# Optimization experiments

Hardware: AMD Instinct MI355X
Metric: run time of the kernel (lower is better)

The kernel has to match this reference:

```python
import jax, jax.numpy as jnp
import numpy as np

CLAMP_LO, CLAMP_HI, CLAMP_GATE_MAX = -10.0, 10.0, 10.0
E, TOPK = 8, 2
M, K, N = 2048, 2048, 1408  # tokens, hidden_dim, intermediate_dim
CAPACITY = 2 * (M * TOPK // E)


def setup_inputs() -> dict:
    key = jax.random.key(0)
    ks = jax.random.split(key, 6)
    bk = 1.0 / np.sqrt(K)  # kaiming_uniform(a=sqrt(5)) bound = 1/sqrt(fan_in)
    bn = 1.0 / np.sqrt(N)
    return {
        "flat_h": jax.random.normal(ks[0], (M, K), jnp.float32),
        "flat_idx": jax.random.randint(ks[1], (M, TOPK), 0, E),
        "flat_gate": jax.random.uniform(ks[2], (M, TOPK), jnp.float32),
        "gate_weight": jax.random.uniform(ks[3], (E, N, K), jnp.float32, -bk, bk),
        "up_weight": jax.random.uniform(ks[4], (E, N, K), jnp.float32, -bk, bk),
        "down_weight": jax.random.uniform(ks[5], (E, K, N), jnp.float32, -bn, bn),
    }


def reference(flat_h, flat_idx, flat_gate, gate_weight, up_weight, down_weight):
    m, top_k = flat_idx.shape
    k = flat_h.shape[1]
    e = gate_weight.shape[0]
    r = m * top_k

    expert_id = flat_idx.reshape(-1)                                   # (R,)
    gate = flat_gate.reshape(-1)                                       # (R,)
    token_index = jnp.repeat(jnp.arange(m, dtype=jnp.int32), top_k)    # (R,)

    # stable sort rows by expert id (mirrors torch.argsort(..., stable=True))
    sort_idx = jnp.argsort(expert_id, stable=True)
    sorted_eid = expert_id[sort_idx]
    tok_sorted = token_index[sort_idx]
    gate_sorted = gate[sort_idx]

    # position of each sorted row inside its expert group
    counts = jnp.bincount(expert_id, length=e)
    starts = jnp.concatenate([jnp.zeros(1, counts.dtype), jnp.cumsum(counts)[:-1]])
    pos = jnp.arange(r) - starts[sorted_eid]                           # (R,)

    # dispatch: scatter sorted tokens into fixed-capacity (E, C, K) buffer
    buf = jnp.zeros((e, CAPACITY, k), flat_h.dtype)
    buf = buf.at[sorted_eid, pos].set(flat_h[tok_sorted])

    # grouped GEMMs: weights stored (E, out, in) like nn.Linear
    g = jnp.einsum("eck,enk->ecn", buf, gate_weight)
    g = jnp.minimum(g, CLAMP_GATE_MAX)
    u = jnp.clip(jnp.einsum("eck,enk->ecn", buf, up_weight), CLAMP_LO, CLAMP_HI)
    h = jax.nn.silu(g) * u                                             # SwiGLU (E, C, N)
    d = jnp.einsum("ecn,ekn->eck", h, down_weight)                     # (E, C, K)

    # combine: gather each routed row back, weight by gate, sum over top_k slots
    expert_out = d[sorted_eid, pos]                                    # (R, K)
    weighted = expert_out * gate_sorted[:, None]
    out = jnp.zeros((m, k), flat_h.dtype).at[tok_sorted].add(weighted)
    return out
```

## Files before the change

### kernel.cpp

```cpp
#include <hip/hip_runtime.h>

#define M_TOK 2048
#define KDIM 2048
#define NDIM 1408
#define NEXP 8
#define RROWS (M_TOK * 2)
#define CAP 1024

typedef __attribute__((ext_vector_type(8))) short short8;
typedef __attribute__((ext_vector_type(4))) float f32x4;

__device__ __forceinline__ unsigned short bf16rn(float f) {
    unsigned int u = __builtin_bit_cast(unsigned int, f);
    u += 0x7FFFu + ((u >> 16) & 1u);
    return (unsigned short)(u >> 16);
}
__device__ __forceinline__ unsigned int pk2(float a, float b) {
    return (unsigned int)bf16rn(a) | ((unsigned int)bf16rn(b) << 16);
}

__device__ __forceinline__ void glds16(const void* g, void* l) {
    __builtin_amdgcn_global_load_lds(
        (const __attribute__((address_space(1))) unsigned int*)g,
        (__attribute__((address_space(3))) unsigned int*)l, 16, 0, 0);
}

__global__ void k_route(const float* __restrict__ h, const int* __restrict__ idx,
                        int* __restrict__ cnt, int* __restrict__ slot_of,
                        unsigned short* __restrict__ bufA) {
    int r = blockIdx.x;
    __shared__ int s_ep;
    if (threadIdx.x == 0) {
        int e = idx[r];
        int p = atomicAdd(&cnt[e], 1);
        int ep = e * CAP + p;
        slot_of[r] = ep;
        s_ep = ep;
    }
    __syncthreads();
    int ep = s_ep;
    const float4* src = (const float4*)(h + (size_t)(r >> 1) * KDIM) + threadIdx.x * 2;
    float4 a = src[0], b = src[1];
    uint4 o;
    o.x = pk2(a.x, a.y); o.y = pk2(a.z, a.w);
    o.z = pk2(b.x, b.y); o.w = pk2(b.z, b.w);
    *((uint4*)(bufA + (size_t)ep * KDIM) + threadIdx.x) = o;
}

__global__ void k_cvt3(const float* __restrict__ s0, const float* __restrict__ s1,
                       const float* __restrict__ s2,
                       unsigned short* __restrict__ d0, unsigned short* __restrict__ d1,
                       unsigned short* __restrict__ d2) {
    const float* src = blockIdx.y == 0 ? s0 : (blockIdx.y == 1 ? s1 : s2);
    unsigned short* dst = blockIdx.y == 0 ? d0 : (blockIdx.y == 1 ? d1 : d2);
    int i = blockIdx.x * blockDim.x + threadIdx.x;
    const float4* s = (const float4*)src + (size_t)i * 2;
    float4 a = s[0], b = s[1];
    uint4 o;
    o.x = pk2(a.x, a.y); o.y = pk2(a.z, a.w);
    o.z = pk2(b.x, b.y); o.w = pk2(b.z, b.w);
    ((uint4*)dst)[i] = o;
}

__global__ __launch_bounds__(256, 2)
void k_gemm1(const unsigned short* __restrict__ bufA,
             const unsigned short* __restrict__ gwb,
             const unsigned short* __restrict__ uwb,
             const int* __restrict__ cnt, unsigned short* __restrict__ hbuf) {
    const int f = blockIdx.x;
    const int e = f & 7;
    const int t = f >> 3;
    const int n_blk = t % 11;
    const int m_blk = t / 11;
    const int m0 = m_blk * 128;
    if (m0 >= cnt[e]) return;
    const int n0 = n_blk * 128;

    const unsigned short* A = bufA + (size_t)e * CAP * KDIM;
    const unsigned short* G = gwb + (size_t)e * NDIM * KDIM;
    const unsigned short* U = uwb + (size_t)e * NDIM * KDIM;

    __shared__ unsigned short sA[128 * 64];
    __shared__ unsigned short sG[128 * 64];
    __shared__ unsigned short sU[128 * 64];

    const int tid = threadIdx.x;
    const int lane = tid & 63;
    const int wave = tid >> 6;
    const int wm = (wave >> 1) * 64, wn = (wave & 1) * 64;
    const int q = lane >> 4, l15 = lane & 15;
    const int sr = lane >> 3;
    const int scb = (lane & 7) ^ (sr & 7);
    const int xi = l15 & 7;
    const int cbl0 = (q ^ xi) * 8;
    const int cbl1 = ((4 + q) ^ xi) * 8;

    f32x4 accG[4][4] = {};
    f32x4 accU[4][4] = {};

    for (int k0 = 0; k0 < KDIM; k0 += 64) {
        __syncthreads();
#pragma unroll
        for (int c = 0; c < 4; c++) {
            int seg = wave * 4 + c;
            int row = seg * 8 + sr;
            glds16(A + (size_t)(m0 + row) * KDIM + k0 + scb * 8, &sA[seg * 512]);
            glds16(G + (size_t)(n0 + row) * KDIM + k0 + scb * 8, &sG[seg * 512]);
            glds16(U + (size_t)(n0 + row) * KDIM + k0 + scb * 8, &sU[seg * 512]);
        }
        __syncthreads();

#pragma unroll
        for (int kh = 0; kh < 2; kh++) {
            const int co = kh ? cbl1 : cbl0;
            short8 af[4], gf[4], uf[4];
#pragma unroll
            for (int i = 0; i < 4; i++) {
                af[i] = *(const short8*)&sA[(wm + i * 16 + l15) * 64 + co];
                gf[i] = *(const short8*)&sG[(wn + i * 16 + l15) * 64 + co];
                uf[i] = *(const short8*)&sU[(wn + i * 16 + l15) * 64 + co];
            }
#pragma unroll
            for (int i = 0; i < 4; i++)
#pragma unroll
                for (int j = 0; j < 4; j++) {
                    accG[i][j] = __builtin_amdgcn_mfma_f32_16x16x32_bf16(af[i], gf[j], accG[i][j], 0, 0, 0);
                    accU[i][j] = __builtin_amdgcn_mfma_f32_16x16x32_bf16(af[i], uf[j], accU[i][j], 0, 0, 0);
                }
        }
    }

    unsigned short* H = hbuf + (size_t)e * CAP * NDIM;
#pragma unroll
    for (int i = 0; i < 4; i++)
#pragma unroll
        for (int j = 0; j < 4; j++) {
            int col = n0 + wn + j * 16 + l15;
#pragma unroll
            for (int rg = 0; rg < 4; rg++) {
                int row = m0 + wm + i * 16 + q * 4 + rg;
                float g = accG[i][j][rg];
                float u = accU[i][j][rg];
                g = fminf(g, 10.f);
                u = fminf(fmaxf(u, -10.f), 10.f);
                float hv = g / (1.f + __expf(-g)) * u;
                H[(size_t)row * NDIM + col] = bf16rn(hv);
            }
        }
}

__global__ __launch_bounds__(256, 2)
void k_gemm2(const unsigned short* __restrict__ hbuf,
             const unsigned short* __restrict__ dwb, const int* __restrict__ cnt,
             float* __restrict__ dbuf) {
    const int f = blockIdx.x;
    const int e = f & 7;
    const int t = f >> 3;
    const int n_blk = t & 15;
    const int m_blk = t >> 4;
    const int cnt_e = cnt[e];
    const int m0 = m_blk * 128;
    if (m0 >= cnt_e) return;
    const int n0 = n_blk * 128;

    const unsigned short* A = hbuf + (size_t)e * CAP * NDIM;
    const unsigned short* B = dwb + (size_t)e * KDIM * NDIM;

    __shared__ unsigned short sA[128 * 64];
    __shared__ unsigned short sB[128 * 64];

    const int tid = threadIdx.x;
    const int lane = tid & 63;
    const int wave = tid >> 6;
    const int wm = (wave >> 1) * 64, wn = (wave & 1) * 64;
    const int q = lane >> 4, l15 = lane & 15;
    const int sr = lane >> 3;
    const int scb = (lane & 7) ^ (sr & 7);
    const int xi = l15 & 7;
    const int cbl0 = (q ^ xi) * 8;
    const int cbl1 = ((4 + q) ^ xi) * 8;

    f32x4 acc[4][4] = {};

    for (int k0 = 0; k0 < NDIM; k0 += 64) {
        __syncthreads();
#pragma unroll
        for (int c = 0; c < 4; c++) {
            int seg = wave * 4 + c;
            int row = seg * 8 + sr;
            glds16(A + (size_t)(m0 + row) * NDIM + k0 + scb * 8, &sA[seg * 512]);
            glds16(B + (size_t)(n0 + row) * NDIM + k0 + scb * 8, &sB[seg * 512]);
        }
        __syncthreads();

#pragma unroll
        for (int kh = 0; kh < 2; kh++) {
            const int co = kh ? cbl1 : cbl0;
            short8 af[4], bfr[4];
#pragma unroll
            for (int i = 0; i < 4; i++) {
                af[i] = *(const short8*)&sA[(wm + i * 16 + l15) * 64 + co];
                bfr[i] = *(const short8*)&sB[(wn + i * 16 + l15) * 64 + co];
            }
#pragma unroll
            for (int i = 0; i < 4; i++)
#pragma unroll
                for (int j = 0; j < 4; j++)
                    acc[i][j] = __builtin_amdgcn_mfma_f32_16x16x32_bf16(af[i], bfr[j], acc[i][j], 0, 0, 0);
        }
    }

    float* D = dbuf + (size_t)e * CAP * KDIM;
#pragma unroll
    for (int i = 0; i < 4; i++) {
#pragma unroll
        for (int rg = 0; rg < 4; rg++) {
            int row = m0 + wm + i * 16 + q * 4 + rg;
            if (row < cnt_e) {
                float* drow = D + (size_t)row * KDIM + n0 + wn + l15;
#pragma unroll
                for (int j = 0; j < 4; j++)
                    drow[j * 16] = acc[i][j][rg];
            }
        }
    }
}

__global__ void k_combine(const float* __restrict__ dbuf, const int* __restrict__ slot_of,
                          const float* __restrict__ gate, float* __restrict__ out) {
    int tk = blockIdx.x;
    int s0 = slot_of[2 * tk], s1 = slot_of[2 * tk + 1];
    float g0 = gate[2 * tk], g1 = gate[2 * tk + 1];
    const float4* r0 = (const float4*)(dbuf + (size_t)s0 * KDIM);
    const float4* r1 = (const float4*)(dbuf + (size_t)s1 * KDIM);
    float4* o = (float4*)(out + (size_t)tk * KDIM);
    int i = threadIdx.x * 2;
#pragma unroll
    for (int c = 0; c < 2; c++) {
        float4 a = r0[i + c], b = r1[i + c];
        float4 v;
        v.x = g0 * a.x + g1 * b.x;
        v.y = g0 * a.y + g1 * b.y;
        v.z = g0 * a.z + g1 * b.z;
        v.w = g0 * a.w + g1 * b.w;
        o[i + c] = v;
    }
}

extern "C" void kernel_launch(void* const* d_in, const int* in_sizes, int n_in,
                              void* d_out, int out_size, void* d_ws, size_t ws_size,
                              hipStream_t stream) {
    const float* flat_h = (const float*)d_in[0];
    const int* flat_idx = (const int*)d_in[1];
    const float* flat_gate = (const float*)d_in[2];
    const float* gw = (const float*)d_in[3];
    const float* uw = (const float*)d_in[4];
    const float* dwn = (const float*)d_in[5];
    float* out = (float*)d_out;

    char* w = (char*)d_ws;
    int* cnt = (int*)w;
    int* slot_of = (int*)(w + 256);
    unsigned short* bufA = (unsigned short*)(w + 1048576ull);
    unsigned short* hbuf = (unsigned short*)(w + 34603008ull);
    unsigned short* gwb  = (unsigned short*)(w + 57671680ull);
    unsigned short* uwb  = (unsigned short*)(w + 103809024ull);
    unsigned short* dwb  = (unsigned short*)(w + 149946368ull);
    float* dbuf = (float*)(w + 57671680ull);

    hipMemsetAsync(cnt, 0, 256, stream);

    const int welems8 = NEXP * NDIM * KDIM / 8;
    k_cvt3<<<dim3(welems8 / 256, 3), 256, 0, stream>>>(gw, uw, dwn, gwb, uwb, dwb);
    k_route<<<RROWS, 256, 0, stream>>>(flat_h, flat_idx, cnt, slot_of, bufA);
    k_gemm1<<<8 * 11 * 8, 256, 0, stream>>>(bufA, gwb, uwb, cnt, hbuf);
    k_gemm2<<<8 * 16 * 8, 256, 0, stream>>>(hbuf, dwb, cnt, dbuf);
    k_combine<<<M_TOK, 256, 0, stream>>>(dbuf, slot_of, flat_gate, out);
}
```

Before: 462.2 us.

## Fuse fp32-to-bf16 weight conversion into grouped GEMM tile loads

Removes the standalone weight conversion kernel and has both GEMM kernels load fp32 weights directly, converting to bf16 in registers before writing swizzled tiles to LDS. This avoids a full read-write pass over all expert weights. In exchange, each m-block reads fp32 weights (double the bytes per reuse), loses the async global-to-LDS path for weights, and raises register pressure.

```diff
diff --git a/kernel.cpp b/kernel.cpp
--- a/kernel.cpp
+++ b/kernel.cpp
@@ -1,4 +1,5 @@
 #include <hip/hip_runtime.h>
+#include <hip/hip_bf16.h>
 
 #define M_TOK 2048
 #define KDIM 2048
@@ -17,6 +18,12 @@
 }
 __device__ __forceinline__ unsigned int pk2(float a, float b) {
     return (unsigned int)bf16rn(a) | ((unsigned int)bf16rn(b) << 16);
+}
+__device__ __forceinline__ unsigned int cvtpk(float a, float b) {
+    __hip_bfloat162 h = __float22bfloat162_rn(make_float2(a, b));
+    unsigned int u;
+    __builtin_memcpy(&u, &h, 4);
+    return u;
 }
 
 __device__ __forceinline__ void glds16(const void* g, void* l) {
@@ -47,25 +54,10 @@
     *((uint4*)(bufA + (size_t)ep * KDIM) + threadIdx.x) = o;
 }
 
-__global__ void k_cvt3(const float* __restrict__ s0, const float* __restrict__ s1,
-                       const float* __restrict__ s2,
-                       unsigned short* __restrict__ d0, unsigned short* __restrict__ d1,
-                       unsigned short* __restrict__ d2) {
-    const float* src = blockIdx.y == 0 ? s0 : (blockIdx.y == 1 ? s1 : s2);
-    unsigned short* dst = blockIdx.y == 0 ? d0 : (blockIdx.y == 1 ? d1 : d2);
-    int i = blockIdx.x * blockDim.x + threadIdx.x;
-    const float4* s = (const float4*)src + (size_t)i * 2;
-    float4 a = s[0], b = s[1];
-    uint4 o;
-    o.x = pk2(a.x, a.y); o.y = pk2(a.z, a.w);
-    o.z = pk2(b.x, b.y); o.w = pk2(b.z, b.w);
-    ((uint4*)dst)[i] = o;
-}
-
 __global__ __launch_bounds__(256, 2)
 void k_gemm1(const unsigned short* __restrict__ bufA,
-             const unsigned short* __restrict__ gwb,
-             const unsigned short* __restrict__ uwb,
+             const float* __restrict__ gw,
+             const float* __restrict__ uw,
              const int* __restrict__ cnt, unsigned short* __restrict__ hbuf) {
     const int f = blockIdx.x;
     const int e = f & 7;
@@ -77,8 +69,8 @@
     const int n0 = n_blk * 128;
 
     const unsigned short* A = bufA + (size_t)e * CAP * KDIM;
-    const unsigned short* G = gwb + (size_t)e * NDIM * KDIM;
-    const unsigned short* U = uwb + (size_t)e * NDIM * KDIM;
+    const float* G = gw + (size_t)e * NDIM * KDIM;
+    const float* U = uw + (size_t)e * NDIM * KDIM;
 
     __shared__ unsigned short sA[128 * 64];
     __shared__ unsigned short sG[128 * 64];
@@ -95,18 +87,50 @@
     const int cbl0 = (q ^ xi) * 8;
     const int cbl1 = ((4 + q) ^ xi) * 8;
 
+    const int wrow = tid >> 1;
+    const int wh = tid & 1;
+    const int wx = wrow & 7;
+    const float* gsrc0 = G + (size_t)(n0 + wrow) * KDIM + wh * 32;
+    const float* usrc0 = U + (size_t)(n0 + wrow) * KDIM + wh * 32;
+    unsigned short* wdG = &sG[wrow * 64];
+    unsigned short* wdU = &sU[wrow * 64];
+
     f32x4 accG[4][4] = {};
     f32x4 accU[4][4] = {};
 
     for (int k0 = 0; k0 < KDIM; k0 += 64) {
+        const float4* gs = (const float4*)(gsrc0 + k0);
+        const float4* us = (const float4*)(usrc0 + k0);
+        float4 gv[8], uv[8];
+#pragma unroll
+        for (int i = 0; i < 8; i++) gv[i] = gs[i];
+#pragma unroll
+        for (int i = 0; i < 8; i++) uv[i] = us[i];
+
         __syncthreads();
 #pragma unroll
         for (int c = 0; c < 4; c++) {
             int seg = wave * 4 + c;
             int row = seg * 8 + sr;
             glds16(A + (size_t)(m0 + row) * KDIM + k0 + scb * 8, &sA[seg * 512]);
-            glds16(G + (size_t)(n0 + row) * KDIM + k0 + scb * 8, &sG[seg * 512]);
-            glds16(U + (size_t)(n0 + row) * KDIM + k0 + scb * 8, &sU[seg * 512]);
+        }
+#pragma unroll
+        for (int g = 0; g < 4; g++) {
+            uint4 o;
+            o.x = cvtpk(gv[2 * g].x, gv[2 * g].y);
+            o.y = cvtpk(gv[2 * g].z, gv[2 * g].w);
+            o.z = cvtpk(gv[2 * g + 1].x, gv[2 * g + 1].y);
+            o.w = cvtpk(gv[2 * g + 1].z, gv[2 * g + 1].w);
+            *(uint4*)(wdG + (((wh * 4 + g) ^ wx) * 8)) = o;
+        }
+#pragma unroll
+        for (int g = 0; g < 4; g++) {
+            uint4 o;
+            o.x = cvtpk(uv[2 * g].x, uv[2 * g].y);
+            o.y = cvtpk(uv[2 * g].z, uv[2 * g].w);
+            o.z = cvtpk(uv[2 * g + 1].x, uv[2 * g + 1].y);
+            o.w = cvtpk(uv[2 * g + 1].z, uv[2 * g + 1].w);
+            *(uint4*)(wdU + (((wh * 4 + g) ^ wx) * 8)) = o;
         }
         __syncthreads();
 
@@ -151,7 +175,7 @@
 
 __global__ __launch_bounds__(256, 2)
 void k_gemm2(const unsigned short* __restrict__ hbuf,
-             const unsigned short* __restrict__ dwb, const int* __restrict__ cnt,
+             const float* __restrict__ dwn, const int* __restrict__ cnt,
              float* __restrict__ dbuf) {
     const int f = blockIdx.x;
     const int e = f & 7;
@@ -164,7 +188,7 @@
     const int n0 = n_blk * 128;
 
     const unsigned short* A = hbuf + (size_t)e * CAP * NDIM;
-    const unsigned short* B = dwb + (size_t)e * KDIM * NDIM;
+    const float* B = dwn + (size_t)e * KDIM * NDIM;
 
     __shared__ unsigned short sA[128 * 64];
     __shared__ unsigned short sB[128 * 64];
@@ -180,16 +204,35 @@
     const int cbl0 = (q ^ xi) * 8;
     const int cbl1 = ((4 + q) ^ xi) * 8;
 
+    const int wrow = tid >> 1;
+    const int wh = tid & 1;
+    const int wx = wrow & 7;
+    const float* bsrc0 = B + (size_t)(n0 + wrow) * NDIM + wh * 32;
+    unsigned short* wdB = &sB[wrow * 64];
+
     f32x4 acc[4][4] = {};
 
     for (int k0 = 0; k0 < NDIM; k0 += 64) {
+        const float4* bs = (const float4*)(bsrc0 + k0);
+        float4 bv[8];
+#pragma unroll
+        for (int i = 0; i < 8; i++) bv[i] = bs[i];
+
         __syncthreads();
 #pragma unroll
         for (int c = 0; c < 4; c++) {
             int seg = wave * 4 + c;
             int row = seg * 8 + sr;
             glds16(A + (size_t)(m0 + row) * NDIM + k0 + scb * 8, &sA[seg * 512]);
-            glds16(B + (size_t)(n0 + row) * NDIM + k0 + scb * 8, &sB[seg * 512]);
+        }
+#pragma unroll
+        for (int g = 0; g < 4; g++) {
+            uint4 o;
+            o.x = cvtpk(bv[2 * g].x, bv[2 * g].y);
+            o.y = cvtpk(bv[2 * g].z, bv[2 * g].w);
+            o.z = cvtpk(bv[2 * g + 1].x, bv[2 * g + 1].y);
+            o.w = cvtpk(bv[2 * g + 1].z, bv[2 * g + 1].w);
+            *(uint4*)(wdB + (((wh * 4 + g) ^ wx) * 8)) = o;
         }
         __syncthreads();
 
@@ -263,17 +306,12 @@
     int* slot_of = (int*)(w + 256);
     unsigned short* bufA = (unsigned short*)(w + 1048576ull);
     unsigned short* hbuf = (unsigned short*)(w + 34603008ull);
-    unsigned short* gwb  = (unsigned short*)(w + 57671680ull);
-    unsigned short* uwb  = (unsigned short*)(w + 103809024ull);
-    unsigned short* dwb  = (unsigned short*)(w + 149946368ull);
     float* dbuf = (float*)(w + 57671680ull);
 
     hipMemsetAsync(cnt, 0, 256, stream);
 
-    const int welems8 = NEXP * NDIM * KDIM / 8;
-    k_cvt3<<<dim3(welems8 / 256, 3), 256, 0, stream>>>(gw, uw, dwn, gwb, uwb, dwb);
     k_route<<<RROWS, 256, 0, stream>>>(flat_h, flat_idx, cnt, slot_of, bufA);
-    k_gemm1<<<8 * 11 * 8, 256, 0, stream>>>(bufA, gwb, uwb, cnt, hbuf);
-    k_gemm2<<<8 * 16 * 8, 256, 0, stream>>>(hbuf, dwb, cnt, dbuf);
+    k_gemm1<<<8 * 11 * 8, 256, 0, stream>>>(bufA, gw, uw, cnt, hbuf);
+    k_gemm2<<<8 * 16 * 8, 256, 0, stream>>>(hbuf, dwn, cnt, dbuf);
     k_combine<<<M_TOK, 256, 0, stream>>>(dbuf, slot_of, flat_gate, out);
 }
```

Measured after the change: 531.5 us. 15.0% more time.

## Double-buffer GEMM LDS loads, shrink N tiles, and pre-tile weights into K-chunks

Applied to the files above, without the earlier changes.

The weight conversion kernel is replaced by a reorder kernel that converts weights to bf16 and also lays them out as contiguous 64-wide K-chunks. Both grouped GEMMs now double-buffer shared memory, issuing the next chunk's global-to-LDS loads before computing the current one, with one barrier per iteration. The N tile is halved to 64 so twice as many blocks run, and gemm2 now targets 3 blocks per CU. The goal is to hide load latency and raise occupancy, at the cost of more A-tile reloads and lower MFMA reuse per block.

```diff
diff --git a/kernel.cpp b/kernel.cpp
--- a/kernel.cpp
+++ b/kernel.cpp
@@ -1,4 +1,5 @@
 #include <hip/hip_runtime.h>
+#include <hip/hip_bf16.h>
 
 #define M_TOK 2048
 #define KDIM 2048
@@ -17,6 +18,12 @@
 }
 __device__ __forceinline__ unsigned int pk2(float a, float b) {
     return (unsigned int)bf16rn(a) | ((unsigned int)bf16rn(b) << 16);
+}
+__device__ __forceinline__ unsigned int cvtpk(float a, float b) {
+    __hip_bfloat162 h = __float22bfloat162_rn(make_float2(a, b));
+    unsigned int u;
+    __builtin_memcpy(&u, &h, 4);
+    return u;
 }
 
 __device__ __forceinline__ void glds16(const void* g, void* l) {
@@ -47,19 +54,28 @@
     *((uint4*)(bufA + (size_t)ep * KDIM) + threadIdx.x) = o;
 }
 
-__global__ void k_cvt3(const float* __restrict__ s0, const float* __restrict__ s1,
-                       const float* __restrict__ s2,
-                       unsigned short* __restrict__ d0, unsigned short* __restrict__ d1,
-                       unsigned short* __restrict__ d2) {
-    const float* src = blockIdx.y == 0 ? s0 : (blockIdx.y == 1 ? s1 : s2);
-    unsigned short* dst = blockIdx.y == 0 ? d0 : (blockIdx.y == 1 ? d1 : d2);
-    int i = blockIdx.x * blockDim.x + threadIdx.x;
-    const float4* s = (const float4*)src + (size_t)i * 2;
-    float4 a = s[0], b = s[1];
-    uint4 o;
-    o.x = pk2(a.x, a.y); o.y = pk2(a.z, a.w);
-    o.z = pk2(b.x, b.y); o.w = pk2(b.z, b.w);
-    ((uint4*)dst)[i] = o;
+__global__ __launch_bounds__(256)
+void k_reorder(const float* __restrict__ in, unsigned short* __restrict__ out,
+               int R, int C) {
+    const int e = blockIdx.x;
+    const int slab = blockIdx.y;
+    const int span = blockIdx.z;
+    const int NC = C >> 6;
+    const int tid = threadIdx.x;
+    const int wave = tid >> 6, lane = tid & 63;
+    const int c = span * 256 + lane * 4;
+    if (c >= C) return;
+    const int r0 = slab * 64 + wave * 16;
+    const float* src = in + ((size_t)e * R + r0) * C + c;
+    unsigned short* dst = out + (((size_t)e * NC + (c >> 6)) * R + r0) * 64 + (c & 63);
+#pragma unroll
+    for (int i = 0; i < 16; i++) {
+        float4 v = *(const float4*)(src + (size_t)i * C);
+        uint2 o;
+        o.x = cvtpk(v.x, v.y);
+        o.y = cvtpk(v.z, v.w);
+        *(uint2*)(dst + i * 64) = o;
+    }
 }
 
 __global__ __launch_bounds__(256, 2)
@@ -70,24 +86,24 @@
     const int f = blockIdx.x;
     const int e = f & 7;
     const int t = f >> 3;
-    const int n_blk = t % 11;
-    const int m_blk = t / 11;
+    const int n_blk = t % 22;
+    const int m_blk = t / 22;
     const int m0 = m_blk * 128;
     if (m0 >= cnt[e]) return;
-    const int n0 = n_blk * 128;
+    const int n0 = n_blk * 64;
 
     const unsigned short* A = bufA + (size_t)e * CAP * KDIM;
-    const unsigned short* G = gwb + (size_t)e * NDIM * KDIM;
-    const unsigned short* U = uwb + (size_t)e * NDIM * KDIM;
-
-    __shared__ unsigned short sA[128 * 64];
-    __shared__ unsigned short sG[128 * 64];
-    __shared__ unsigned short sU[128 * 64];
+    const unsigned short* Gc = gwb + (size_t)e * 32 * NDIM * 64;
+    const unsigned short* Uc = uwb + (size_t)e * 32 * NDIM * 64;
+
+    __shared__ unsigned short sA[2][128 * 64];
+    __shared__ unsigned short sG[2][64 * 64];
+    __shared__ unsigned short sU[2][64 * 64];
 
     const int tid = threadIdx.x;
     const int lane = tid & 63;
     const int wave = tid >> 6;
-    const int wm = (wave >> 1) * 64, wn = (wave & 1) * 64;
+    const int wm = (wave >> 1) * 64, wn = (wave & 1) * 32;
     const int q = lane >> 4, l15 = lane & 15;
     const int sr = lane >> 3;
     const int scb = (lane & 7) ^ (sr & 7);
@@ -95,46 +111,64 @@
     const int cbl0 = (q ^ xi) * 8;
     const int cbl1 = ((4 + q) ^ xi) * 8;
 
-    f32x4 accG[4][4] = {};
-    f32x4 accU[4][4] = {};
-
-    for (int k0 = 0; k0 < KDIM; k0 += 64) {
-        __syncthreads();
-#pragma unroll
-        for (int c = 0; c < 4; c++) {
-            int seg = wave * 4 + c;
-            int row = seg * 8 + sr;
-            glds16(A + (size_t)(m0 + row) * KDIM + k0 + scb * 8, &sA[seg * 512]);
-            glds16(G + (size_t)(n0 + row) * KDIM + k0 + scb * 8, &sG[seg * 512]);
-            glds16(U + (size_t)(n0 + row) * KDIM + k0 + scb * 8, &sU[seg * 512]);
-        }
-        __syncthreads();
+    f32x4 accG[4][2] = {};
+    f32x4 accU[4][2] = {};
+
+#define STAGE1(kc, b) do {                                                              \
+        _Pragma("unroll")                                                               \
+        for (int c_ = 0; c_ < 4; c_++) {                                                \
+            int seg = wave * 4 + c_;                                                    \
+            glds16(A + (size_t)(m0 + seg * 8 + sr) * KDIM + (kc) * 64 + scb * 8,        \
+                   &sA[b][seg * 512]);                                                  \
+        }                                                                               \
+        _Pragma("unroll")                                                               \
+        for (int c_ = 0; c_ < 2; c_++) {                                                \
+            int seg = wave * 2 + c_;                                                    \
+            glds16(Gc + ((size_t)(kc) * NDIM + n0 + seg * 8 + sr) * 64 + scb * 8,       \
+                   &sG[b][seg * 512]);                                                  \
+            glds16(Uc + ((size_t)(kc) * NDIM + n0 + seg * 8 + sr) * 64 + scb * 8,       \
+                   &sU[b][seg * 512]);                                                  \
+        }                                                                               \
+    } while (0)
+
+    STAGE1(0, 0);
+
+    for (int kc = 0; kc < 32; kc++) {
+        const int cur = kc & 1;
+        asm volatile("s_waitcnt vmcnt(0)" ::: "memory");
+        __builtin_amdgcn_sched_barrier(0);
+        __builtin_amdgcn_s_barrier();
+        __builtin_amdgcn_sched_barrier(0);
+        if (kc + 1 < 32) STAGE1(kc + 1, cur ^ 1);
 
 #pragma unroll
         for (int kh = 0; kh < 2; kh++) {
             const int co = kh ? cbl1 : cbl0;
-            short8 af[4], gf[4], uf[4];
-#pragma unroll
-            for (int i = 0; i < 4; i++) {
-                af[i] = *(const short8*)&sA[(wm + i * 16 + l15) * 64 + co];
-                gf[i] = *(const short8*)&sG[(wn + i * 16 + l15) * 64 + co];
-                uf[i] = *(const short8*)&sU[(wn + i * 16 + l15) * 64 + co];
+            short8 af[4], gf[2], uf[2];
+#pragma unroll
+            for (int i = 0; i < 4; i++)
+                af[i] = *(const short8*)&sA[cur][(wm + i * 16 + l15) * 64 + co];
+#pragma unroll
+            for (int j = 0; j < 2; j++) {
+                gf[j] = *(const short8*)&sG[cur][(wn + j * 16 + l15) * 64 + co];
+                uf[j] = *(const short8*)&sU[cur][(wn + j * 16 + l15) * 64 + co];
             }
 #pragma unroll
             for (int i = 0; i < 4; i++)
 #pragma unroll
-                for (int j = 0; j < 4; j++) {
+                for (int j = 0; j < 2; j++) {
                     accG[i][j] = __builtin_amdgcn_mfma_f32_16x16x32_bf16(af[i], gf[j], accG[i][j], 0, 0, 0);
                     accU[i][j] = __builtin_amdgcn_mfma_f32_16x16x32_bf16(af[i], uf[j], accU[i][j], 0, 0, 0);
                 }
         }
     }
+#undef STAGE1
 
     unsigned short* H = hbuf + (size_t)e * CAP * NDIM;
 #pragma unroll
     for (int i = 0; i < 4; i++)
 #pragma unroll
-        for (int j = 0; j < 4; j++) {
+        for (int j = 0; j < 2; j++) {
             int col = n0 + wn + j * 16 + l15;
 #pragma unroll
             for (int rg = 0; rg < 4; rg++) {
@@ -149,30 +183,30 @@
         }
 }
 
-__global__ __launch_bounds__(256, 2)
+__global__ __launch_bounds__(256, 3)
 void k_gemm2(const unsigned short* __restrict__ hbuf,
              const unsigned short* __restrict__ dwb, const int* __restrict__ cnt,
              float* __restrict__ dbuf) {
     const int f = blockIdx.x;
     const int e = f & 7;
     const int t = f >> 3;
-    const int n_blk = t & 15;
-    const int m_blk = t >> 4;
+    const int n_blk = t & 31;
+    const int m_blk = t >> 5;
     const int cnt_e = cnt[e];
     const int m0 = m_blk * 128;
     if (m0 >= cnt_e) return;
-    const int n0 = n_blk * 128;
-
-    const unsigned short* A = hbuf + (size_t)e * CAP * NDIM;
-    const unsigned short* B = dwb + (size_t)e * KDIM * NDIM;
-
-    __shared__ unsigned short sA[128 * 64];
-    __shared__ unsigned short sB[128 * 64];
+    const int n0 = n_blk * 64;
+
+    const unsigned short* Ah = hbuf + (size_t)e * CAP * NDIM;
+    const unsigned short* Dc = dwb + (size_t)e * 22 * KDIM * 64;
+
+    __shared__ unsigned short sA[2][128 * 64];
+    __shared__ unsigned short sB[2][64 * 64];
 
     const int tid = threadIdx.x;
     const int lane = tid & 63;
     const int wave = tid >> 6;
-    const int wm = (wave >> 1) * 64, wn = (wave & 1) * 64;
+    const int wm = (wave >> 1) * 64, wn = (wave & 1) * 32;
     const int q = lane >> 4, l15 = lane & 15;
     const int sr = lane >> 3;
     const int scb = (lane & 7) ^ (sr & 7);
@@ -180,35 +214,51 @@
     const int cbl0 = (q ^ xi) * 8;
     const int cbl1 = ((4 + q) ^ xi) * 8;
 
-    f32x4 acc[4][4] = {};
-
-    for (int k0 = 0; k0 < NDIM; k0 += 64) {
-        __syncthreads();
-#pragma unroll
-        for (int c = 0; c < 4; c++) {
-            int seg = wave * 4 + c;
-            int row = seg * 8 + sr;
-            glds16(A + (size_t)(m0 + row) * NDIM + k0 + scb * 8, &sA[seg * 512]);
-            glds16(B + (size_t)(n0 + row) * NDIM + k0 + scb * 8, &sB[seg * 512]);
-        }
-        __syncthreads();
+    f32x4 acc[4][2] = {};
+
+#define STAGE2(nc, b) do {                                                              \
+        _Pragma("unroll")                                                               \
+        for (int c_ = 0; c_ < 4; c_++) {                                                \
+            int seg = wave * 4 + c_;                                                    \
+            glds16(Ah + (size_t)(m0 + seg * 8 + sr) * NDIM + (nc) * 64 + scb * 8,       \
+                   &sA[b][seg * 512]);                                                  \
+        }                                                                               \
+        _Pragma("unroll")                                                               \
+        for (int c_ = 0; c_ < 2; c_++) {                                                \
+            int seg = wave * 2 + c_;                                                    \
+            glds16(Dc + ((size_t)(nc) * KDIM + n0 + seg * 8 + sr) * 64 + scb * 8,       \
+                   &sB[b][seg * 512]);                                                  \
+        }                                                                               \
+    } while (0)
+
+    STAGE2(0, 0);
+
+    for (int nc = 0; nc < 22; nc++) {
+        const int cur = nc & 1;
+        asm volatile("s_waitcnt vmcnt(0)" ::: "memory");
+        __builtin_amdgcn_sched_barrier(0);
+        __builtin_amdgcn_s_barrier();
+        __builtin_amdgcn_sched_barrier(0);
+        if (nc + 1 < 22) STAGE2(nc + 1, cur ^ 1);
 
 #pragma unroll
         for (int kh = 0; kh < 2; kh++) {
             const int co = kh ? cbl1 : cbl0;
-            short8 af[4], bfr[4];
-#pragma unroll
-            for (int i = 0; i < 4; i++) {
-                af[i] = *(const short8*)&sA[(wm + i * 16 + l15) * 64 + co];
-                bfr[i] = *(const short8*)&sB[(wn + i * 16 + l15) * 64 + co];
-            }
+            short8 af[4], bfr[2];
 #pragma unroll
             for (int i = 0; i < 4; i++)
-#pragma unroll
-                for (int j = 0; j < 4; j++)
+                af[i] = *(const short8*)&sA[cur][(wm + i * 16 + l15) * 64 + co];
+#pragma unroll
+            for (int j = 0; j < 2; j++)
+                bfr[j] = *(const short8*)&sB[cur][(wn + j * 16 + l15) * 64 + co];
+#pragma unroll
+            for (int i = 0; i < 4; i++)
+#pragma unroll
+                for (int j = 0; j < 2; j++)
                     acc[i][j] = __builtin_amdgcn_mfma_f32_16x16x32_bf16(af[i], bfr[j], acc[i][j], 0, 0, 0);
         }
     }
+#undef STAGE2
 
     float* D = dbuf + (size_t)e * CAP * KDIM;
 #pragma unroll
@@ -219,7 +269,7 @@
             if (row < cnt_e) {
                 float* drow = D + (size_t)row * KDIM + n0 + wn + l15;
 #pragma unroll
-                for (int j = 0; j < 4; j++)
+                for (int j = 0; j < 2; j++)
                     drow[j * 16] = acc[i][j][rg];
             }
         }
@@ -270,10 +320,11 @@
 
     hipMemsetAsync(cnt, 0, 256, stream);
 
-    const int welems8 = NEXP * NDIM * KDIM / 8;
-    k_cvt3<<<dim3(welems8 / 256, 3), 256, 0, stream>>>(gw, uw, dwn, gwb, uwb, dwb);
     k_route<<<RROWS, 256, 0, stream>>>(flat_h, flat_idx, cnt, slot_of, bufA);
-    k_gemm1<<<8 * 11 * 8, 256, 0, stream>>>(bufA, gwb, uwb, cnt, hbuf);
-    k_gemm2<<<8 * 16 * 8, 256, 0, stream>>>(hbuf, dwb, cnt, dbuf);
+    k_reorder<<<dim3(8, 22, 8), 256, 0, stream>>>(gw, gwb, NDIM, KDIM);
+    k_reorder<<<dim3(8, 22, 8), 256, 0, stream>>>(uw, uwb, NDIM, KDIM);
+    k_reorder<<<dim3(8, 32, 6), 256, 0, stream>>>(dwn, dwb, KDIM, NDIM);
+    k_gemm1<<<8 * 22 * 8, 256, 0, stream>>>(bufA, gwb, uwb, cnt, hbuf);
+    k_gemm2<<<8 * 32 * 8, 256, 0, stream>>>(hbuf, dwb, cnt, dbuf);
     k_combine<<<M_TOK, 256, 0, stream>>>(dbuf, slot_of, flat_gate, out);
 }
```

Measured after the change: 514.6 us. 11.3% more time.
